# Performance work log

Measured on AMD Instinct MI355X. Metric: run time of the kernel, lower is better.

Reference implementation:

```python
import jax, jax.numpy as jnp
import numpy as np

B, C, N, E, F = 8, 4, 2048, 512, 2048
EPS = 1e-5
MASK_SCALE = 5.0


def layer_norm(x, gamma, beta):
    mu = jnp.mean(x, axis=-1, keepdims=True)
    var = jnp.mean(jnp.square(x - mu), axis=-1, keepdims=True)
    return (x - mu) * jax.lax.rsqrt(var + EPS) * gamma + beta


def setup_inputs() -> dict:
    key = jax.random.key(0)
    ks = jax.random.split(key, 8)
    src = jax.random.normal(ks[0], (B, C, N, E), dtype=jnp.float32)
    key_padding_mask = jax.random.uniform(ks[1], (B, N), dtype=jnp.float32)
    # FFN params (torch Linear default init scale ~ U(-1/sqrt(fan_in), +))
    W1 = jax.random.normal(ks[2], (E, F), dtype=jnp.float32) / np.sqrt(E)
    b1 = jnp.zeros((F,), dtype=jnp.float32)
    W2 = jax.random.normal(ks[3], (F, E), dtype=jnp.float32) / np.sqrt(F)
    b2 = jnp.zeros((E,), dtype=jnp.float32)
    g1 = jnp.ones((E,), dtype=jnp.float32)
    be1 = jnp.zeros((E,), dtype=jnp.float32)
    g2 = jnp.ones((E,), dtype=jnp.float32)
    be2 = jnp.zeros((E,), dtype=jnp.float32)
    return {"src": src, "key_padding_mask": key_padding_mask,
            "W1": W1, "b1": b1, "W2": W2, "b2": b2,
            "g1": g1, "be1": be1, "g2": g2, "be2": be2}


def reference(src, key_padding_mask, W1, b1, W2, b2, g1, be1, g2, be2):
    # src: [B, C, N, E]; channels batched into one fused attention call
    scale = 1.0 / jnp.sqrt(jnp.asarray(src.shape[-1], src.dtype))
    scores = jnp.einsum('bcne,bcme->bcnm', src, src) * scale  # [B,C,N,N]
    scores = scores - key_padding_mask[:, None, None, :] * MASK_SCALE
    attn = jax.nn.softmax(scores, axis=-1)
    attn_out = jnp.einsum('bcnm,bcme->bcne', attn, src)
    # residual + norm1 (dropout is identity at eval)
    src2 = layer_norm(src + attn_out, g1, be1)
    # feedforward: Linear -> ReLU -> Linear
    ff = jax.nn.relu(jnp.einsum('bcne,ef->bcnf', src2, W1) + b1)
    ff = jnp.einsum('bcnf,fe->bcne', ff, W2) + b2
    out = layer_norm(src2 + ff, g2, be2)
    return out
```

## Files before the change

kernel.cpp:

```cpp
#include <hip/hip_runtime.h>
#include <stdint.h>

constexpr int CB = 8, CC = 4, CN = 2048, CE = 512, CF = 2048;
constexpr long long TOT = (long long)CB * CC * CN * CE;
constexpr int GRP = 16;
constexpr int MCH = 65536;
constexpr float SCALE = 0.04419417382415922f;
constexpr float MASK_SCALE = 5.0f;
constexpr float EPS = 1e-5f;

typedef unsigned short bf16_t;
typedef __attribute__((ext_vector_type(4))) float f32x4;
typedef __attribute__((ext_vector_type(8))) short s16x8;

#define DEV static __device__ __forceinline__

DEV unsigned short f2bf(float f) {
    unsigned u = __float_as_uint(f);
    unsigned r = (u + 0x7fffu + ((u >> 16) & 1u)) >> 16;
    return (unsigned short)r;
}
DEV float bf2f(unsigned short b) {
    return __uint_as_float(((unsigned)b) << 16);
}

typedef const __attribute__((address_space(1))) unsigned int* gptr_t;
typedef __attribute__((address_space(3))) unsigned int* lptr_t;
DEV void async16(const void* g, void* l) {
    __builtin_amdgcn_global_load_lds((gptr_t)g, (lptr_t)l, 16, 0, 0);
}

#define FULL_BAR() do { asm volatile("" ::: "memory"); __builtin_amdgcn_s_barrier(); asm volatile("" ::: "memory"); } while (0)
#define LGKM0() asm volatile("s_waitcnt lgkmcnt(0)" ::: "memory")
#define VMCNT(N_) asm volatile("s_waitcnt vmcnt(" #N_ ")" ::: "memory")

DEV float blockSum256(float v, float* sm) {
    #pragma unroll
    for (int o = 32; o; o >>= 1) v += __shfl_xor(v, o);
    int w = threadIdx.x >> 6;
    __syncthreads();
    if ((threadIdx.x & 63) == 0) sm[w] = v;
    __syncthreads();
    return sm[0] + sm[1] + sm[2] + sm[3];
}
DEV float blockMax256(float v, float* sm) {
    #pragma unroll
    for (int o = 32; o; o >>= 1) v = fmaxf(v, __shfl_xor(v, o));
    int w = threadIdx.x >> 6;
    __syncthreads();
    if ((threadIdx.x & 63) == 0) sm[w] = v;
    __syncthreads();
    return fmaxf(fmaxf(sm[0], sm[1]), fmaxf(sm[2], sm[3]));
}

__global__ __launch_bounds__(256) void cvt_transpose(
    const float* __restrict__ in, bf16_t* __restrict__ outN,
    bf16_t* __restrict__ outT) {
    __shared__ bf16_t tile[32][33];
    const float* inz = in + (size_t)blockIdx.z * CN * CE;
    bf16_t* oN = outN + (size_t)blockIdx.z * CN * CE;
    bf16_t* oT = outT + (size_t)blockIdx.z * CE * CN;
    int rb = blockIdx.y * 32;
    int cb = blockIdx.x * 32;
    int tx = threadIdx.x & 31, ty = threadIdx.x >> 5;
    #pragma unroll
    for (int i = 0; i < 32; i += 8) {
        float v = inz[(size_t)(rb + ty + i) * CE + cb + tx];
        unsigned short h = f2bf(v);
        oN[(size_t)(rb + ty + i) * CE + cb + tx] = h;
        tile[ty + i][tx] = h;
    }
    __syncthreads();
    #pragma unroll
    for (int i = 0; i < 32; i += 8)
        oT[(size_t)(cb + ty + i) * CN + rb + tx] = tile[tx][ty + i];
}

__global__ __launch_bounds__(256) void transpose_f32_bf16(
    const float* __restrict__ in, bf16_t* __restrict__ out,
    int R, int Cc) {
    __shared__ float tile[32][33];
    int rb = blockIdx.y * 32, cb = blockIdx.x * 32;
    int tx = threadIdx.x & 31, ty = threadIdx.x >> 5;
    #pragma unroll
    for (int i = 0; i < 32; i += 8)
        tile[ty + i][tx] = in[(size_t)(rb + ty + i) * Cc + cb + tx];
    __syncthreads();
    #pragma unroll
    for (int i = 0; i < 32; i += 8)
        out[(size_t)(cb + ty + i) * R + rb + tx] = f2bf(tile[tx][ty + i]);
}

#define GEMM_CORE_DECLS() \
    extern __shared__ bf16_t lds[]; \
    bf16_t* AsL = lds; \
    bf16_t* BsL = lds + 32768; \
    const int t = threadIdx.x; \
    const int lane = t & 63, wid = t >> 6; \
    const int wr = wid >> 2, wc = wid & 3; \
    const int NT = K >> 6; \
    const int r0 = t >> 3, s0 = t & 7; \
    const int ce = ((s0 ^ (r0 & 7)) << 3); \
    const bf16_t* aP0 = Az + (size_t)(brow + r0) * K + ce; \
    const bf16_t* bP0 = Bz + (size_t)(bcol + r0) * K + ce; \
    const size_t rK64 = (size_t)64 * K; \
    const size_t h128K = rK64 * 2; \
    const int q = lane >> 4, rr0 = lane & 15, xmask = rr0 & 7; \
    s16x8 af[4][2]; \
    s16x8 bv[2][2][2]; \
    f32x4 acc[2][2][4][2] = {};

#define STAGE_A(kt_, h_) do { \
    bf16_t* d_ = AsL + ((((kt_) & 1) * 2 + (h_)) * 8192); \
    const bf16_t* s_ = aP0 + (size_t)(h_) * h128K + (size_t)(kt_) * 64; \
    async16(s_, d_ + t * 8); \
    async16(s_ + rK64, d_ + 4096 + t * 8); \
} while (0)
#define STAGE_B(kt_, h_) do { \
    bf16_t* d_ = BsL + ((((kt_) & 1) * 2 + (h_)) * 8192); \
    const bf16_t* s_ = bP0 + (size_t)(h_) * h128K + (size_t)(kt_) * 64; \
    async16(s_, d_ + t * 8); \
    async16(s_ + rK64, d_ + 4096 + t * 8); \
} while (0)
#define READ_A(ktp_, qm_) do { \
    const bf16_t* base_ = AsL + (((ktp_) * 2 + (qm_)) * 8192); \
    _Pragma("unroll") for (int m_ = 0; m_ < 4; ++m_) \
    _Pragma("unroll") for (int ks_ = 0; ks_ < 2; ++ks_) \
        af[m_][ks_] = *(const s16x8*)(base_ + (wr * 64 + m_ * 16 + rr0) * 64 + (((ks_ * 4 + q) ^ xmask) << 3)); \
} while (0)
#define READ_B(ktp_, qn_) do { \
    const bf16_t* base_ = BsL + (((ktp_) * 2 + (qn_)) * 8192); \
    _Pragma("unroll") for (int n_ = 0; n_ < 2; ++n_) \
    _Pragma("unroll") for (int ks_ = 0; ks_ < 2; ++ks_) \
        bv[qn_][n_][ks_] = *(const s16x8*)(base_ + (wc * 32 + n_ * 16 + rr0) * 64 + (((ks_ * 4 + q) ^ xmask) << 3)); \
} while (0)
#define MFMA_Q(qm_, qn_) do { \
    __builtin_amdgcn_s_setprio(1); \
    _Pragma("unroll") for (int m_ = 0; m_ < 4; ++m_) \
    _Pragma("unroll") for (int n_ = 0; n_ < 2; ++n_) \
    _Pragma("unroll") for (int ks_ = 0; ks_ < 2; ++ks_) \
        acc[qm_][qn_][m_][n_] = __builtin_amdgcn_mfma_f32_16x16x32_bf16( \
            af[m_][ks_], bv[qn_][n_][ks_], acc[qm_][qn_][m_][n_], 0, 0, 0); \
    __builtin_amdgcn_s_setprio(0); \
} while (0)

#define GEMM_MAIN_LOOP_8P() \
    STAGE_A(0, 0); STAGE_B(0, 0); STAGE_B(0, 1); STAGE_A(0, 1); \
    if (1 < NT) { \
        STAGE_A(1, 0); STAGE_B(1, 0); \
        VMCNT(4); \
    } else { \
        VMCNT(0); \
    } \
    FULL_BAR(); \
    for (int kt = 0; kt < NT; ++kt) { \
        const int ktp = kt & 1; \
        READ_A(ktp, 0); \
        READ_B(ktp, 0); \
        if (kt + 1 < NT) STAGE_B(kt + 1, 1); \
        FULL_BAR(); \
        LGKM0(); \
        MFMA_Q(0, 0); \
        FULL_BAR(); \
        READ_B(ktp, 1); \
        if (kt + 1 < NT) STAGE_A(kt + 1, 1); \
        FULL_BAR(); \
        LGKM0(); \
        MFMA_Q(0, 1); \
        FULL_BAR(); \
        READ_A(ktp, 1); \
        if (kt + 2 < NT) STAGE_A(kt + 2, 0); \
        FULL_BAR(); \
        LGKM0(); \
        MFMA_Q(1, 0); \
        FULL_BAR(); \
        if (kt + 2 < NT) { \
            STAGE_B(kt + 2, 0); \
            VMCNT(4); \
        } else { \
            VMCNT(0); \
        } \
        FULL_BAR(); \
        MFMA_Q(1, 1); \
        FULL_BAR(); \
    }

#define GEMM_MAIN_LOOP_2P() \
    STAGE_A(0, 0); STAGE_B(0, 0); STAGE_B(0, 1); STAGE_A(0, 1); \
    VMCNT(2); \
    FULL_BAR(); \
    for (int kt = 0; kt < NT; ++kt) { \
        const int ktp = kt & 1; \
        READ_A(ktp, 0); \
        READ_B(ktp, 0); \
        READ_B(ktp, 1); \
        if (kt + 1 < NT) { \
            STAGE_A(kt + 1, 0); STAGE_B(kt + 1, 0); STAGE_B(kt + 1, 1); \
            VMCNT(6); \
        } else { \
            VMCNT(0); \
        } \
        FULL_BAR(); \
        LGKM0(); \
        MFMA_Q(0, 0); \
        MFMA_Q(0, 1); \
        READ_A(ktp, 1); \
        if (kt + 1 < NT) { \
            STAGE_A(kt + 1, 1); \
            VMCNT(2); \
        } \
        FULL_BAR(); \
        LGKM0(); \
        MFMA_Q(1, 0); \
        MFMA_Q(1, 1); \
    }

#define GEMM_EPILOGUE(EPI_) do { \
    size_t cz = (size_t)bz * sC; \
    bf16_t* Cb = (bf16_t*)Cptr + cz; \
    _Pragma("unroll") for (int qm = 0; qm < 2; ++qm) \
    _Pragma("unroll") for (int qn = 0; qn < 2; ++qn) \
    _Pragma("unroll") for (int n = 0; n < 2; ++n) { \
        int col = bcol + qn * 128 + wc * 32 + n * 16 + rr0; \
        float bvv = ((EPI_) == 1 || (EPI_) == 4) ? bias[col] : 0.f; \
        _Pragma("unroll") for (int m = 0; m < 4; ++m) { \
            _Pragma("unroll") for (int j = 0; j < 4; ++j) { \
                float v = acc[qm][qn][m][n][j] + bvv; \
                if ((EPI_) == 1) v = fmaxf(v, 0.f); \
                if ((EPI_) == 3) v *= alpha; \
                int row = brow + qm * 128 + wr * 64 + m * 16 + q * 4 + j; \
                Cb[(size_t)row * Nc + col] = f2bf(v); \
            } \
        } \
    } \
} while (0)

template <int EPI>
__global__ __launch_bounds__(512, 2) void gemm256(
    const bf16_t* __restrict__ A, const bf16_t* __restrict__ B,
    void* __restrict__ Cptr, const float* __restrict__ bias, float alpha,
    int Nc, int K, long long sA, long long sB, long long sC) {
    int bx, by, bz;
    {
        int gx = gridDim.x, gy = gridDim.y;
        int nwg = gx * gy * gridDim.z;
        int flat = blockIdx.x + gx * (blockIdx.y + gy * blockIdx.z);
        int wg = (nwg & 7) ? flat : ((flat & 7) * (nwg >> 3) + (flat >> 3));
        bx = wg % gx;
        int tmp = wg / gx;
        by = tmp % gy;
        bz = tmp / gy;
    }
    const bf16_t* Az = A + (size_t)bz * sA;
    const bf16_t* Bz = B + (size_t)bz * sB;
    const int brow = by * 256, bcol = bx * 256;

    GEMM_CORE_DECLS();
    GEMM_MAIN_LOOP_8P();
    GEMM_EPILOGUE(EPI);
}

template <int EPI>
__global__ __launch_bounds__(512, 2) void gemm256s(
    const bf16_t* __restrict__ A, const bf16_t* __restrict__ B,
    void* __restrict__ Cptr, const float* __restrict__ bias, float alpha,
    int Nc, int K, long long sA, long long sB, long long sC) {
    int bx, by, bz;
    {
        int gx = gridDim.x, gy = gridDim.y;
        int nwg = gx * gy * gridDim.z;
        int flat = blockIdx.x + gx * (blockIdx.y + gy * blockIdx.z);
        int wg = (nwg & 7) ? flat : ((flat & 7) * (nwg >> 3) + (flat >> 3));
        bx = wg % gx;
        int tmp = wg / gx;
        by = tmp % gy;
        bz = tmp / gy;
    }
    const bf16_t* Az = A + (size_t)bz * sA;
    const bf16_t* Bz = B + (size_t)bz * sB;
    const int brow = by * 256, bcol = bx * 256;

    GEMM_CORE_DECLS();
    GEMM_MAIN_LOOP_2P();
    GEMM_EPILOGUE(EPI);
}

__global__ __launch_bounds__(512, 2) void gemm256_sym(
    const bf16_t* __restrict__ A, bf16_t* __restrict__ Cptr, float alpha,
    int Nc, int K, long long sA, long long sC) {
    int bx, by, bz;
    {
        int gx = gridDim.x;
        int nwg = gx * gridDim.z;
        int flat = blockIdx.x + gx * blockIdx.z;
        int wg = (nwg & 7) ? flat : ((flat & 7) * (nwg >> 3) + (flat >> 3));
        int tri = wg % gx;
        bz = wg / gx;
        int i = 0, b = 0;
        while (b + i + 1 <= tri) { b += i + 1; i++; }
        by = i;
        bx = tri - b;
    }
    const bf16_t* Az = A + (size_t)bz * sA;
    const bf16_t* Bz = Az;
    const int brow = by * 256, bcol = bx * 256;

    GEMM_CORE_DECLS();
    GEMM_MAIN_LOOP_2P();

    size_t cz = (size_t)bz * sC;
    bf16_t* Cb = (bf16_t*)Cptr + cz;
    const bool mirror = (bx != by);
    #pragma unroll
    for (int qm = 0; qm < 2; ++qm)
    #pragma unroll
    for (int qn = 0; qn < 2; ++qn)
    #pragma unroll
    for (int n = 0; n < 2; ++n) {
        int col = bcol + qn * 128 + wc * 32 + n * 16 + rr0;
        #pragma unroll
        for (int m = 0; m < 4; ++m) {
            unsigned short hh[4];
            int row0 = brow + qm * 128 + wr * 64 + m * 16 + q * 4;
            #pragma unroll
            for (int j = 0; j < 4; ++j) {
                hh[j] = f2bf(acc[qm][qn][m][n][j] * alpha);
                Cb[(size_t)(row0 + j) * Nc + col] = hh[j];
            }
            if (mirror) {
                ushort4 mv;
                mv.x = hh[0]; mv.y = hh[1]; mv.z = hh[2]; mv.w = hh[3];
                *(ushort4*)&Cb[(size_t)col * Nc + row0] = mv;
            }
        }
    }
}

__global__ __launch_bounds__(256) void softmax_bf16(
    bf16_t* __restrict__ S, const float* __restrict__ mask, int bc0) {
    __shared__ float sm[4];
    int gr = blockIdx.x;
    int b = (bc0 + (gr >> 11)) >> 2;
    bf16_t* row = S + (size_t)gr * CN;
    int tid = threadIdx.x;
    const float* mrow = mask + (size_t)b * CN + tid * 8;
    s16x8 v = *(const s16x8*)(row + tid * 8);
    float4 m0 = *(const float4*)(mrow);
    float4 m1 = *(const float4*)(mrow + 4);
    float x[8];
    x[0] = bf2f((unsigned short)v[0]) - m0.x * MASK_SCALE;
    x[1] = bf2f((unsigned short)v[1]) - m0.y * MASK_SCALE;
    x[2] = bf2f((unsigned short)v[2]) - m0.z * MASK_SCALE;
    x[3] = bf2f((unsigned short)v[3]) - m0.w * MASK_SCALE;
    x[4] = bf2f((unsigned short)v[4]) - m1.x * MASK_SCALE;
    x[5] = bf2f((unsigned short)v[5]) - m1.y * MASK_SCALE;
    x[6] = bf2f((unsigned short)v[6]) - m1.z * MASK_SCALE;
    x[7] = bf2f((unsigned short)v[7]) - m1.w * MASK_SCALE;
    float mx = -3.4e38f;
    #pragma unroll
    for (int i = 0; i < 8; i++) mx = fmaxf(mx, x[i]);
    mx = blockMax256(mx, sm);
    float s = 0.f;
    #pragma unroll
    for (int i = 0; i < 8; i++) { x[i] = __expf(x[i] - mx); s += x[i]; }
    s = blockSum256(s, sm);
    float inv = 1.f / s;
    s16x8 u;
    #pragma unroll
    for (int i = 0; i < 8; i++) u[i] = (short)f2bf(x[i] * inv);
    *(s16x8*)(row + tid * 8) = u;
}

__global__ __launch_bounds__(256) void ln1_kernel(
    const bf16_t* __restrict__ src, const bf16_t* __restrict__ ao,
    const float* __restrict__ g, const float* __restrict__ be,
    bf16_t* __restrict__ o) {
    __shared__ float sm[4];
    size_t base = (size_t)blockIdx.x * CE;
    int e = threadIdx.x * 2;
    ushort2 s = *(const ushort2*)&src[base + e];
    ushort2 a = *(const ushort2*)&ao[base + e];
    float x0 = bf2f(s.x) + bf2f(a.x), x1 = bf2f(s.y) + bf2f(a.y);
    float mu = blockSum256(x0 + x1, sm) * (1.f / CE);
    float d0 = x0 - mu, d1 = x1 - mu;
    float var = blockSum256(d0 * d0 + d1 * d1, sm) * (1.f / CE);
    float rs = rsqrtf(var + EPS);
    ushort2 w;
    w.x = f2bf(d0 * rs * g[e] + be[e]);
    w.y = f2bf(d1 * rs * g[e + 1] + be[e + 1]);
    *(ushort2*)&o[base + e] = w;
}

__global__ __launch_bounds__(256) void ln2_kernel(
    const bf16_t* __restrict__ a, const bf16_t* __restrict__ b,
    const float* __restrict__ g, const float* __restrict__ be,
    float* __restrict__ o) {
    __shared__ float sm[4];
    size_t base = (size_t)blockIdx.x * CE;
    int e = threadIdx.x * 2;
    ushort2 aa = *(const ushort2*)&a[base + e];
    ushort2 bb = *(const ushort2*)&b[base + e];
    float x0 = bf2f(aa.x) + bf2f(bb.x), x1 = bf2f(aa.y) + bf2f(bb.y);
    float mu = blockSum256(x0 + x1, sm) * (1.f / CE);
    float d0 = x0 - mu, d1 = x1 - mu;
    float var = blockSum256(d0 * d0 + d1 * d1, sm) * (1.f / CE);
    float rs = rsqrtf(var + EPS);
    float2 w;
    w.x = d0 * rs * g[e] + be[e];
    w.y = d1 * rs * g[e + 1] + be[e + 1];
    *(float2*)&o[base + e] = w;
}

extern "C" void kernel_launch(void* const* d_in, const int* in_sizes, int n_in,
                              void* d_out, int out_size, void* d_ws, size_t ws_size,
                              hipStream_t stream) {
    const float* src  = (const float*)d_in[0];
    const float* mask = (const float*)d_in[1];
    const float* W1   = (const float*)d_in[2];
    const float* b1   = (const float*)d_in[3];
    const float* W2   = (const float*)d_in[4];
    const float* b2   = (const float*)d_in[5];
    const float* g1   = (const float*)d_in[6];
    const float* be1  = (const float*)d_in[7];
    const float* g2   = (const float*)d_in[8];
    const float* be2  = (const float*)d_in[9];
    float* out = (float*)d_out;
    char* ws = (char*)d_ws;

    hipFuncSetAttribute(reinterpret_cast<const void*>(&gemm256<3>), hipFuncAttributeMaxDynamicSharedMemorySize, 131072);
    hipFuncSetAttribute(reinterpret_cast<const void*>(&gemm256<4>), hipFuncAttributeMaxDynamicSharedMemorySize, 131072);
    hipFuncSetAttribute(reinterpret_cast<const void*>(&gemm256s<1>), hipFuncAttributeMaxDynamicSharedMemorySize, 131072);
    hipFuncSetAttribute(reinterpret_cast<const void*>(&gemm256_sym), hipFuncAttributeMaxDynamicSharedMemorySize, 131072);

    const size_t MB = 1024 * 1024;
    bf16_t* probs  = (bf16_t*)(ws);
    bf16_t* src_bf = (bf16_t*)(ws + 256 * MB);
    bf16_t* srcT   = (bf16_t*)(ws + 320 * MB);
    bf16_t* attnO  = (bf16_t*)(ws + 384 * MB);
    bf16_t* W1T    = (bf16_t*)(ws + 448 * MB);
    bf16_t* W2T    = (bf16_t*)(ws + 450 * MB);
    bf16_t* src2   = (bf16_t*)(ws);
    bf16_t* ff     = (bf16_t*)(ws + 64 * MB);
    bf16_t* H      = (bf16_t*)(ws + 128 * MB);
    if (ws_size < 452 * MB) return;

    cvt_transpose<<<dim3(CE / 32, CN / 32, 32), 256, 0, stream>>>(src, src_bf, srcT);
    transpose_f32_bf16<<<dim3(CF / 32, CE / 32, 1), 256, 0, stream>>>(W1, W1T, CE, CF);
    transpose_f32_bf16<<<dim3(CE / 32, CF / 32, 1), 256, 0, stream>>>(W2, W2T, CF, CE);

    gemm256_sym<<<dim3(36, 1, 32), 512, 131072, stream>>>(
        src_bf, probs, SCALE, CN, CE,
        (long long)CN * CE, (long long)CN * CN);
    for (int g0 = 0; g0 < CB * CC; g0 += GRP) {
        bf16_t* probs_g = probs + (size_t)g0 * CN * CN;
        softmax_bf16<<<dim3(GRP * CN), 256, 0, stream>>>(probs_g, mask, g0);
        gemm256<3><<<dim3(CE / 256, CN / 256, GRP), 512, 131072, stream>>>(
            probs_g, srcT + (size_t)g0 * CE * CN, attnO + (size_t)g0 * CN * CE,
            nullptr, 1.0f, CE, CN,
            (long long)CN * CN, (long long)CE * CN, (long long)CN * CE);
    }
    ln1_kernel<<<dim3(CB * CC * CN), 256, 0, stream>>>(src_bf, attnO, g1, be1, src2);

    gemm256s<1><<<dim3(CF / 256, MCH / 256, 1), 512, 131072, stream>>>(
        src2, W1T, H, b1, 1.0f, CF, CE, 0, 0, 0);
    gemm256<4><<<dim3(CE / 256, MCH / 256, 1), 512, 131072, stream>>>(
        H, W2T, ff, b2, 1.0f, CE, CF, 0, 0, 0);
    ln2_kernel<<<dim3(MCH), 256, 0, stream>>>(src2, ff, g2, be2, out);
}
```

Measured before the change: 857.1 us.

## Fuse second FFN GEMM with bias, residual and LayerNorm2 epilogue

Replaces the FFN2 GEMM plus the separate ln2 kernel with one kernel. Each block computes a full 128x512 output row tile, so the row statistics can be reduced in-block and the normalized fp32 output written directly. This removes the bf16 round trip of the ff intermediate and a launch. In exchange the tiles are narrower on M (128 rows, 512 blocks), which may reduce GEMM efficiency, and the variance is now computed as E[x^2]-mu^2.

```diff
diff --git a/kernel.cpp b/kernel.cpp
--- a/kernel.cpp
+++ b/kernel.cpp
@@ -32,6 +32,7 @@
 
 #define FULL_BAR() do { asm volatile("" ::: "memory"); __builtin_amdgcn_s_barrier(); asm volatile("" ::: "memory"); } while (0)
 #define LGKM0() asm volatile("s_waitcnt lgkmcnt(0)" ::: "memory")
+#define SCHED0() __builtin_amdgcn_sched_barrier(0)
 #define VMCNT(N_) asm volatile("s_waitcnt vmcnt(" #N_ ")" ::: "memory")
 
 DEV float blockSum256(float v, float* sm) {
@@ -336,6 +337,117 @@
     }
 }
 
+__global__ __launch_bounds__(512, 1) void gemm_ffn2_ln(
+    const bf16_t* __restrict__ A, const bf16_t* __restrict__ B,
+    float* __restrict__ Out, const float* __restrict__ bias,
+    const bf16_t* __restrict__ R, const float* __restrict__ g,
+    const float* __restrict__ be, int K) {
+    extern __shared__ bf16_t lds[];
+    const int t = threadIdx.x;
+    const int lane = t & 63, wid = t >> 6;
+    const int wr = wid >> 2, wc = wid & 3;
+    const int by = blockIdx.y;
+    const int NT = K >> 5;
+
+    const int r0 = t >> 2, s0 = t & 3;
+    const int qsrc = s0 ^ ((r0 >> 1) & 3);
+    const bf16_t* aP = A + (size_t)(by * 128 + r0) * K + qsrc * 8;
+    const bf16_t* bP = B + (size_t)r0 * K + qsrc * 8;
+    const size_t r128K = (size_t)128 * K;
+
+    #define FP_PUSH(kt_, p_) do { \
+        bf16_t* ab_ = lds + (p_) * 20480; \
+        const bf16_t* sa_ = aP + (size_t)(kt_) * 32; \
+        async16(sa_, ab_ + t * 8); \
+        bf16_t* bb_ = ab_ + 4096; \
+        const bf16_t* sb_ = bP + (size_t)(kt_) * 32; \
+        async16(sb_, bb_ + t * 8); \
+        async16(sb_ + r128K, bb_ + 4096 + t * 8); \
+        async16(sb_ + 2 * r128K, bb_ + 8192 + t * 8); \
+        async16(sb_ + 3 * r128K, bb_ + 12288 + t * 8); \
+    } while (0)
+
+    const int q = lane >> 4, rr0 = lane & 15;
+    f32x4 acc[4][8] = {};
+
+    FP_PUSH(0, 0);
+    FP_PUSH(1, 1);
+    VMCNT(5);
+    FULL_BAR();
+
+    for (int i = 0; i < NT; ++i) {
+        const int p = i % 3;
+        const bf16_t* Ab = lds + p * 20480;
+        const bf16_t* Bb = Ab + 4096;
+        s16x8 af[4], bv[8];
+        #pragma unroll
+        for (int m = 0; m < 4; ++m) {
+            int row = wr * 64 + m * 16 + rr0;
+            af[m] = *(const s16x8*)(Ab + row * 32 + ((q ^ ((row >> 1) & 3)) << 3));
+        }
+        #pragma unroll
+        for (int n = 0; n < 8; ++n) {
+            int row = wc * 128 + n * 16 + rr0;
+            bv[n] = *(const s16x8*)(Bb + row * 32 + ((q ^ ((row >> 1) & 3)) << 3));
+        }
+        if (i + 2 < NT) FP_PUSH(i + 2, (i + 2) % 3);
+        LGKM0(); SCHED0();
+        __builtin_amdgcn_s_setprio(1);
+        #pragma unroll
+        for (int m = 0; m < 4; ++m)
+            #pragma unroll
+            for (int n = 0; n < 8; ++n)
+                acc[m][n] = __builtin_amdgcn_mfma_f32_16x16x32_bf16(af[m], bv[n], acc[m][n], 0, 0, 0);
+        __builtin_amdgcn_s_setprio(0);
+        if (i + 2 < NT) { VMCNT(5); } else { VMCNT(0); }
+        FULL_BAR();
+    }
+
+    float* parts = (float*)lds;
+    const int colb = wc * 128;
+    const size_t rowBase = (size_t)by * 128;
+    #pragma unroll
+    for (int m = 0; m < 4; ++m) {
+        #pragma unroll
+        for (int j = 0; j < 4; ++j) {
+            int r = wr * 64 + m * 16 + q * 4 + j;
+            const bf16_t* Rrow = R + (rowBase + r) * 512;
+            float s1 = 0.f, s2 = 0.f;
+            #pragma unroll
+            for (int n = 0; n < 8; ++n) {
+                int col = colb + n * 16 + rr0;
+                float x = acc[m][n][j] + bias[col] + bf2f(Rrow[col]);
+                s1 += x; s2 += x * x;
+            }
+            #pragma unroll
+            for (int o = 8; o; o >>= 1) { s1 += __shfl_xor(s1, o); s2 += __shfl_xor(s2, o); }
+            if (rr0 == 0) { parts[r * 8 + wc * 2] = s1; parts[r * 8 + wc * 2 + 1] = s2; }
+        }
+    }
+    __syncthreads();
+    #pragma unroll
+    for (int m = 0; m < 4; ++m) {
+        #pragma unroll
+        for (int j = 0; j < 4; ++j) {
+            int r = wr * 64 + m * 16 + q * 4 + j;
+            float s1 = parts[r * 8] + parts[r * 8 + 2] + parts[r * 8 + 4] + parts[r * 8 + 6];
+            float s2 = parts[r * 8 + 1] + parts[r * 8 + 3] + parts[r * 8 + 5] + parts[r * 8 + 7];
+            float mu = s1 * (1.f / 512);
+            float var = s2 * (1.f / 512) - mu * mu;
+            float rs = rsqrtf(var + EPS);
+            const bf16_t* Rrow = R + (rowBase + r) * 512;
+            float* Orow = Out + (rowBase + r) * 512;
+            #pragma unroll
+            for (int n = 0; n < 8; ++n) {
+                int col = colb + n * 16 + rr0;
+                float x = acc[m][n][j] + bias[col] + bf2f(Rrow[col]);
+                Orow[col] = (x - mu) * rs * g[col] + be[col];
+            }
+        }
+    }
+    #undef FP_PUSH
+}
+
 __global__ __launch_bounds__(256) void softmax_bf16(
     bf16_t* __restrict__ S, const float* __restrict__ mask, int bc0) {
     __shared__ float sm[4];
@@ -391,26 +503,6 @@
     *(ushort2*)&o[base + e] = w;
 }
 
-__global__ __launch_bounds__(256) void ln2_kernel(
-    const bf16_t* __restrict__ a, const bf16_t* __restrict__ b,
-    const float* __restrict__ g, const float* __restrict__ be,
-    float* __restrict__ o) {
-    __shared__ float sm[4];
-    size_t base = (size_t)blockIdx.x * CE;
-    int e = threadIdx.x * 2;
-    ushort2 aa = *(const ushort2*)&a[base + e];
-    ushort2 bb = *(const ushort2*)&b[base + e];
-    float x0 = bf2f(aa.x) + bf2f(bb.x), x1 = bf2f(aa.y) + bf2f(bb.y);
-    float mu = blockSum256(x0 + x1, sm) * (1.f / CE);
-    float d0 = x0 - mu, d1 = x1 - mu;
-    float var = blockSum256(d0 * d0 + d1 * d1, sm) * (1.f / CE);
-    float rs = rsqrtf(var + EPS);
-    float2 w;
-    w.x = d0 * rs * g[e] + be[e];
-    w.y = d1 * rs * g[e + 1] + be[e + 1];
-    *(float2*)&o[base + e] = w;
-}
-
 extern "C" void kernel_launch(void* const* d_in, const int* in_sizes, int n_in,
                               void* d_out, int out_size, void* d_ws, size_t ws_size,
                               hipStream_t stream) {
@@ -428,9 +520,9 @@
     char* ws = (char*)d_ws;
 
     hipFuncSetAttribute(reinterpret_cast<const void*>(&gemm256<3>), hipFuncAttributeMaxDynamicSharedMemorySize, 131072);
-    hipFuncSetAttribute(reinterpret_cast<const void*>(&gemm256<4>), hipFuncAttributeMaxDynamicSharedMemorySize, 131072);
     hipFuncSetAttribute(reinterpret_cast<const void*>(&gemm256s<1>), hipFuncAttributeMaxDynamicSharedMemorySize, 131072);
     hipFuncSetAttribute(reinterpret_cast<const void*>(&gemm256_sym), hipFuncAttributeMaxDynamicSharedMemorySize, 131072);
+    hipFuncSetAttribute(reinterpret_cast<const void*>(&gemm_ffn2_ln), hipFuncAttributeMaxDynamicSharedMemorySize, 122880);
 
     const size_t MB = 1024 * 1024;
     bf16_t* probs  = (bf16_t*)(ws);
@@ -440,7 +532,6 @@
     bf16_t* W1T    = (bf16_t*)(ws + 448 * MB);
     bf16_t* W2T    = (bf16_t*)(ws + 450 * MB);
     bf16_t* src2   = (bf16_t*)(ws);
-    bf16_t* ff     = (bf16_t*)(ws + 64 * MB);
     bf16_t* H      = (bf16_t*)(ws + 128 * MB);
     if (ws_size < 452 * MB) return;
 
@@ -463,7 +554,6 @@
 
     gemm256s<1><<<dim3(CF / 256, MCH / 256, 1), 512, 131072, stream>>>(
         src2, W1T, H, b1, 1.0f, CF, CE, 0, 0, 0);
-    gemm256<4><<<dim3(CE / 256, MCH / 256, 1), 512, 131072, stream>>>(
-        H, W2T, ff, b2, 1.0f, CE, CF, 0, 0, 0);
-    ln2_kernel<<<dim3(MCH), 256, 0, stream>>>(src2, ff, g2, be2, out);
-}
+    gemm_ffn2_ln<<<dim3(1, MCH / 128, 1), 512, 122880, stream>>>(
+        H, W2T, out, b2, src2, g2, be2, CF);
+}
```

Result: no change. 868.9 us (+1.4%).
